# Optimization experiments

Hardware: AMD Instinct MI355X
Metric: run time of the kernel (lower is better)

## Reference

```python
import jax, jax.numpy as jnp
import numpy as np

SLOPE = 25.0   # snntorch surrogate.fast_sigmoid default slope
THR = 1.0      # snntorch Leaky default threshold
BETA = 0.95
SPIKE_STEPS = 4
NUM_HEADS = 16

@jax.custom_vjp
def spike(u):
    # Heaviside forward, fast-sigmoid surrogate backward
    return (u > 0).astype(u.dtype)

def _spike_fwd(u):
    return spike(u), u

def _spike_bwd(u, g):
    return (g / (SLOPE * jnp.abs(u) + 1.0) ** 2,)

spike.defvjp(_spike_fwd, _spike_bwd)

def lif_mean(cur):
    """Run SPIKE_STEPS of a snntorch Leaky neuron (subtract reset, detached)
    with constant input current `cur`; return mean spike train over time."""
    def step(mem, _):
        reset = jax.lax.stop_gradient(spike(mem - THR))
        mem = BETA * mem + cur - reset * THR
        return mem, spike(mem - THR)
    _, spk = jax.lax.scan(step, jnp.zeros_like(cur), None, length=SPIKE_STEPS)
    return spk.mean(axis=0)

def setup_inputs() -> dict:
    B, S, D = 2, 2048, 1024
    key = jax.random.key(0)
    ks = jax.random.split(key, 9)
    std = 1.0 / np.sqrt(D)
    mkw = lambda k: jax.random.uniform(k, (D, D), jnp.float32, -std, std)
    mkb = lambda k: jax.random.uniform(k, (D,), jnp.float32, -std, std)
    return {
        "x": jax.random.normal(ks[0], (B, S, D), jnp.float32),
        "q_w": mkw(ks[1]), "q_b": mkb(ks[2]),
        "k_w": mkw(ks[3]), "k_b": mkb(ks[4]),
        "v_w": mkw(ks[5]), "v_b": mkb(ks[6]),
        "o_w": mkw(ks[7]), "o_b": mkb(ks[8]),
    }

def reference(x, q_w, q_b, k_w, k_b, v_w, v_b, o_w, o_b):
    B, S, D = x.shape
    H = NUM_HEADS
    Hd = D // H
    # projections -> [B, H, S, Hd]  (weights stored [in, out])
    proj = lambda w, b: (x @ w + b).reshape(B, S, H, Hd).transpose(0, 2, 1, 3)
    q, k, v = proj(q_w, q_b), proj(k_w, k_b), proj(v_w, v_b)
    # LIF spiking recurrence, aggregated over time
    q_agg, k_agg, v_agg = lif_mean(q), lif_mean(k), lif_mean(v)
    # standard scaled dot-product attention on aggregated spikes
    scores = jnp.einsum('bhqd,bhkd->bhqk', q_agg, k_agg) / jnp.sqrt(jnp.float32(Hd))
    attn = jax.nn.softmax(scores, axis=-1)
    out = jnp.einsum('bhqk,bhkd->bhqd', attn, v_agg)
    out = out.transpose(0, 2, 1, 3).reshape(B, S, D)
    return out @ o_w + o_b
```

## Files before the change

kernel.cpp:

```cpp
#include <hip/hip_runtime.h>
#include <hip/hip_bf16.h>
#include <stdint.h>

typedef unsigned short u16;
typedef unsigned int u32;
typedef __bf16 bf16x8 __attribute__((ext_vector_type(8)));
typedef float f32x4 __attribute__((ext_vector_type(4)));

#define B_   2
#define S_   2048
#define D_   1024
#define H_   16
#define HD_  64

__device__ __forceinline__ u16 f2bf(float f) {
    u32 u = __float_as_uint(f);
    u32 r = (u + 0x7FFFu + ((u >> 16) & 1u)) >> 16;
    return (u16)r;
}
__device__ __forceinline__ float bf2f(u16 s) { return __uint_as_float(((u32)s) << 16); }

__device__ __forceinline__ f32x4 mfma16(bf16x8 a, bf16x8 b, f32x4 c) {
    return __builtin_amdgcn_mfma_f32_16x16x32_bf16(a, b, c, 0, 0, 0);
}

__device__ __forceinline__ void gl16(const u16* g, u16* l) {
    __builtin_amdgcn_global_load_lds(
        (const __attribute__((address_space(1))) void*)g,
        (__attribute__((address_space(3))) void*)l, 16, 0, 0);
}

__global__ void prep_kernel(const float* __restrict__ x,
                            const float* __restrict__ qw, const float* __restrict__ kw,
                            const float* __restrict__ vw, const float* __restrict__ ow,
                            u16* __restrict__ xbf, u16* __restrict__ wt_all) {
    __shared__ float tile[32][33];
    const int bid = blockIdx.x;
    const int t = threadIdx.x;
    if (bid < 4096) {
        int i = bid * 256 + t;
        float4 v = reinterpret_cast<const float4*>(x)[i];
        uint2 hp;
        hp.x = (u32)f2bf(v.x) | ((u32)f2bf(v.y) << 16);
        hp.y = (u32)f2bf(v.z) | ((u32)f2bf(v.w) << 16);
        reinterpret_cast<uint2*>(xbf)[i] = hp;
        return;
    }
    const int f = bid - 4096;
    const int z = f >> 10;
    const int bi = (f & 1023) >> 5;
    const int bj = f & 31;
    const float* w = (z == 0) ? qw : (z == 1) ? kw : (z == 2) ? vw : ow;
    u16* thi = wt_all + (size_t)z * 1048576;
    const int tx = t & 31, ty = t >> 5;
#pragma unroll
    for (int k = 0; k < 4; k++) {
        int r = ty + k * 8;
        tile[r][tx] = w[(size_t)(bi * 32 + r) * D_ + bj * 32 + tx];
    }
    __syncthreads();
#pragma unroll
    for (int k = 0; k < 4; k++) {
        int r = ty + k * 8;
        thi[(size_t)(bj * 32 + r) * D_ + bi * 32 + tx] = f2bf(tile[tx][r]);
    }
}

__global__ __launch_bounds__(256, 3)
void qkv_gemm(const u16* __restrict__ Ag, const u16* __restrict__ Bg,
              const float* __restrict__ qb, const float* __restrict__ kb,
              const float* __restrict__ vb,
              u16* __restrict__ o0, u16* __restrict__ o1, u16* __restrict__ o2) {
    __shared__ __align__(16) u16 lA[2][128 * 32];
    __shared__ __align__(16) u16 lB[2][128 * 32];

    const int t = threadIdx.x;
    const int flat = blockIdx.y * 24 + blockIdx.x;
    const int swz = (flat & 7) * 96 + (flat >> 3);
    const int m0 = (swz / 24) * 128;
    const int n0 = (swz % 24) * 128;
    const int wid = t >> 6, lane = t & 63;
    const int wm = wid >> 1, wn = wid & 1;
    const int lr = lane & 15, lg = lane >> 4;

    f32x4 acc[4][4] = {};

    auto STAGE = [&](int buf, int kk) {
        const int k0 = kk * 32;
#pragma unroll
        for (int p = 0; p < 2; p++) {
            int idx = p * 256 + wid * 64 + lane;
            int row = idx >> 2, sl = idx & 3;
            int slx = sl ^ ((row >> 1) & 3);
            gl16(Ag + (size_t)(m0 + row) * D_ + k0 + slx * 8,
                 &lA[buf][(p * 256 + wid * 64) * 8]);
            gl16(Bg + (size_t)(n0 + row) * D_ + k0 + slx * 8,
                 &lB[buf][(p * 256 + wid * 64) * 8]);
        }
    };

    STAGE(0, 0);
    __syncthreads();
    int cur = 0;

    for (int kk = 0; kk < 32; ++kk) {
        if (kk < 31) STAGE(cur ^ 1, kk + 1);

        bf16x8 af[4], bf[4];
#pragma unroll
        for (int m = 0; m < 4; m++) {
            int row = wm * 64 + m * 16 + lr;
            af[m] = *reinterpret_cast<const bf16x8*>(
                &lA[cur][row * 32 + (lg ^ ((row >> 1) & 3)) * 8]);
        }
#pragma unroll
        for (int n = 0; n < 4; n++) {
            int row = wn * 64 + n * 16 + lr;
            bf[n] = *reinterpret_cast<const bf16x8*>(
                &lB[cur][row * 32 + (lg ^ ((row >> 1) & 3)) * 8]);
        }
#pragma unroll
        for (int m = 0; m < 4; m++)
#pragma unroll
            for (int n = 0; n < 4; n++)
                acc[m][n] = mfma16(af[m], bf[n], acc[m][n]);

        __syncthreads();
        cur ^= 1;
    }

    const int col0f = n0 + wn * 64;
    const int proj = col0f >> 10;
    const float* bp = (proj == 0) ? qb : (proj == 1) ? kb : vb;
    u16* dst = (proj == 0) ? o0 : (proj == 1) ? o1 : o2;
#pragma unroll
    for (int m = 0; m < 4; m++) {
#pragma unroll
        for (int n = 0; n < 4; n++) {
            u16 agg4[4];
#pragma unroll
            for (int r = 0; r < 4; r++) {
                int row = m0 + wm * 64 + m * 16 + lg * 4 + r;
                int colp = (col0f + n * 16 + lr) & 1023;
                float cur_i = acc[m][n][r] + bp[colp];
                float mem = 0.f;
                int cnt = 0;
#pragma unroll
                for (int tt = 0; tt < 4; tt++) {
                    float reset = (mem > 1.f) ? 1.f : 0.f;
                    mem = 0.95f * mem;
                    mem = mem + cur_i;
                    mem = mem - reset;
                    cnt += (mem > 1.f) ? 1 : 0;
                }
                u16 agg = (u16)(__float_as_uint((float)cnt * 0.25f) >> 16);
                if (proj != 2) {
                    int b = row >> 11, s = row & 2047;
                    int h = colp >> 6, d = colp & 63;
                    dst[((size_t)(b * H_ + h) * S_ + s) * HD_ + d] = agg;
                } else {
                    agg4[r] = agg;
                }
            }
            if (proj == 2) {
                int row0 = m0 + wm * 64 + m * 16 + lg * 4;
                int colp = (col0f + n * 16 + lr) & 1023;
                int b = row0 >> 11, s = row0 & 2047;
                int h = colp >> 6, d = colp & 63;
                uint2 pk;
                pk.x = (u32)agg4[0] | ((u32)agg4[1] << 16);
                pk.y = (u32)agg4[2] | ((u32)agg4[3] << 16);
                *reinterpret_cast<uint2*>(
                    &dst[((size_t)(b * H_ + h) * HD_ + d) * S_ + s]) = pk;
            }
        }
    }
}

__global__ __launch_bounds__(256, 4)
void o_gemm(const u16* __restrict__ Ag, const u16* __restrict__ Bhg,
            const float* __restrict__ bias, float* __restrict__ out) {
    __shared__ __align__(16) u16 lA[2][64 * 32];
    __shared__ __align__(16) u16 lB[2][64 * 32];

    const int t = threadIdx.x;
    const int flat = blockIdx.y * 16 + blockIdx.x;
    const int swz = (flat & 7) * 128 + (flat >> 3);
    const int m0 = (swz >> 4) * 64;
    const int n0 = (swz & 15) * 64;
    const int wid = t >> 6, lane = t & 63;
    const int wm = wid >> 1, wn = wid & 1;
    const int lr = lane & 15, lg = lane >> 4;

    f32x4 acc[2][2] = {};

    auto STAGE = [&](int buf, int kk) {
        const int k0 = kk * 32;
        int idx = wid * 64 + lane;
        int row = idx >> 2, sl = idx & 3;
        int slx = sl ^ ((row >> 1) & 3);
        gl16(Ag + (size_t)(m0 + row) * D_ + k0 + slx * 8,
             &lA[buf][(wid * 64) * 8]);
        gl16(Bhg + (size_t)(n0 + row) * D_ + k0 + slx * 8,
             &lB[buf][(wid * 64) * 8]);
    };

    STAGE(0, 0);
    __syncthreads();
    int cur = 0;

    for (int kk = 0; kk < 32; ++kk) {
        if (kk < 31) STAGE(cur ^ 1, kk + 1);

        bf16x8 af[2], bf[2];
#pragma unroll
        for (int m = 0; m < 2; m++) {
            int row = wm * 32 + m * 16 + lr;
            af[m] = *reinterpret_cast<const bf16x8*>(
                &lA[cur][row * 32 + (lg ^ ((row >> 1) & 3)) * 8]);
        }
#pragma unroll
        for (int n = 0; n < 2; n++) {
            int row = wn * 32 + n * 16 + lr;
            bf[n] = *reinterpret_cast<const bf16x8*>(
                &lB[cur][row * 32 + (lg ^ ((row >> 1) & 3)) * 8]);
        }
#pragma unroll
        for (int m = 0; m < 2; m++)
#pragma unroll
            for (int n = 0; n < 2; n++)
                acc[m][n] = mfma16(af[m], bf[n], acc[m][n]);

        __syncthreads();
        cur ^= 1;
    }

#pragma unroll
    for (int m = 0; m < 2; m++)
#pragma unroll
        for (int n = 0; n < 2; n++)
#pragma unroll
            for (int r = 0; r < 4; r++) {
                int row = m0 + wm * 32 + m * 16 + lg * 4 + r;
                int col = n0 + wn * 32 + n * 16 + lr;
                out[(size_t)row * D_ + col] = acc[m][n][r] + bias[col];
            }
}

__global__ __launch_bounds__(256, 2)
void attn_kernel(const u16* __restrict__ qa, const u16* __restrict__ ka,
                 const u16* __restrict__ vt, u16* __restrict__ oag) {
    __shared__ __align__(16) u16 Kb[2][2][64 * 64];
    __shared__ __align__(16) u16 Vb[2][2][64 * 64];
    __shared__ __align__(16) u16 Pt[4][32 * 64];

    const int t = threadIdx.x;
    const int wid = t >> 6, lane = t & 63;
    const int lr = lane & 15, lg = lane >> 4;

    const int flat = blockIdx.y * 16 + blockIdx.x;
    const int swz = (flat & 7) * 64 + (flat >> 3);
    const int bh = swz >> 4;
    const int q0 = (swz & 15) * 128;

    const u16* qbase = qa + (size_t)bh * S_ * HD_;
    const u16* kbase = ka + (size_t)bh * S_ * HD_;
    const u16* vbase = vt + (size_t)bh * HD_ * S_;

    bf16x8 qf[2][2];
#pragma unroll
    for (int m = 0; m < 2; m++)
#pragma unroll
        for (int kc = 0; kc < 2; kc++) {
            int row = q0 + wid * 32 + m * 16 + lr;
            qf[m][kc] = *reinterpret_cast<const bf16x8*>(
                qbase + (size_t)row * HD_ + kc * 32 + lg * 8);
        }

    bf16x8 ones;
#pragma unroll
    for (int j = 0; j < 8; j++) ones[j] = (__bf16)1.0f;

    f32x4 oacc[2][4] = {};
    f32x4 ssum[2] = {};
    u16* myP = &Pt[wid][0];

    auto STAGE = [&](int buf, int kt2) {
#pragma unroll
        for (int s = 0; s < 2; s++) {
#pragma unroll
            for (int p = 0; p < 2; p++) {
                int slot = p * 256 + wid * 64 + lane;
                int row = slot >> 3, sl = slot & 7;
                int slx = sl ^ (row & 7);
                gl16(kbase + (size_t)((kt2 + s) * 64 + row) * HD_ + slx * 8,
                     &Kb[buf][s][(p * 256 + wid * 64) * 8]);
                gl16(vbase + (size_t)row * S_ + (kt2 + s) * 64 + slx * 8,
                     &Vb[buf][s][(p * 256 + wid * 64) * 8]);
            }
        }
    };

    auto COMPUTE = [&](const u16* Kt, const u16* Vt) {
        f32x4 sacc[2][4] = {};
        __builtin_amdgcn_s_setprio(1);
#pragma unroll
        for (int n = 0; n < 4; n++) {
            int row = n * 16 + lr;
#pragma unroll
            for (int kc = 0; kc < 2; kc++) {
                int sl = kc * 4 + lg;
                bf16x8 kb = *reinterpret_cast<const bf16x8*>(
                    &Kt[row * 64 + ((sl ^ (row & 7)) * 8)]);
                sacc[0][n] = mfma16(qf[0][kc], kb, sacc[0][n]);
                sacc[1][n] = mfma16(qf[1][kc], kb, sacc[1][n]);
            }
        }
        __builtin_amdgcn_s_setprio(0);
        char* pbase = reinterpret_cast<char*>(myP);
#pragma unroll
        for (int m = 0; m < 2; m++)
#pragma unroll
            for (int n = 0; n < 4; n++) {
                float pv[4];
#pragma unroll
                for (int r = 0; r < 4; r++) {
                    float tt = __builtin_fmaf(sacc[m][n][r], 0.18033688f,
                                              -5.7707802f);
                    asm("v_exp_f32 %0, %1" : "=v"(pv[r]) : "v"(tt));
                }
                u32 d01, d23;
                asm("v_cvt_pk_bf16_f32 %0, %1, %2"
                    : "=v"(d01) : "v"(pv[0]), "v"(pv[1]));
                asm("v_cvt_pk_bf16_f32 %0, %1, %2"
                    : "=v"(d23) : "v"(pv[2]), "v"(pv[3]));
                const int pr = m * 16 + lg * 4;
                const int cb = (n * 16 + lr) * 2;
                *reinterpret_cast<u16*>(pbase + (pr + 0) * 128 +
                                        (cb ^ (((pr + 0) & 7) << 4))) = (u16)d01;
                *reinterpret_cast<u16*>(pbase + (pr + 1) * 128 +
                                        (cb ^ (((pr + 1) & 7) << 4))) = (u16)(d01 >> 16);
                *reinterpret_cast<u16*>(pbase + (pr + 2) * 128 +
                                        (cb ^ (((pr + 2) & 7) << 4))) = (u16)d23;
                *reinterpret_cast<u16*>(pbase + (pr + 3) * 128 +
                                        (cb ^ (((pr + 3) & 7) << 4))) = (u16)(d23 >> 16);
            }
        bf16x8 pa[2][2];
#pragma unroll
        for (int m = 0; m < 2; m++)
#pragma unroll
            for (int kc = 0; kc < 2; kc++) {
                int row = m * 16 + lr;
                int sl = kc * 4 + lg;
                pa[m][kc] = *reinterpret_cast<const bf16x8*>(
                    &myP[row * 64 + ((sl ^ (row & 7)) * 8)]);
            }
        __builtin_amdgcn_s_setprio(1);
#pragma unroll
        for (int n = 0; n < 4; n++) {
            int row = n * 16 + lr;
#pragma unroll
            for (int kc = 0; kc < 2; kc++) {
                int sl = kc * 4 + lg;
                bf16x8 vb = *reinterpret_cast<const bf16x8*>(
                    &Vt[row * 64 + ((sl ^ (row & 7)) * 8)]);
                oacc[0][n] = mfma16(pa[0][kc], vb, oacc[0][n]);
                oacc[1][n] = mfma16(pa[1][kc], vb, oacc[1][n]);
            }
        }
        ssum[0] = mfma16(pa[0][0], ones, ssum[0]);
        ssum[0] = mfma16(pa[0][1], ones, ssum[0]);
        ssum[1] = mfma16(pa[1][0], ones, ssum[1]);
        ssum[1] = mfma16(pa[1][1], ones, ssum[1]);
        __builtin_amdgcn_s_setprio(0);
    };

    STAGE(0, 0);
    __syncthreads();
    int cur = 0;

    for (int pt = 0; pt < 16; ++pt) {
        if (pt < 15) STAGE(cur ^ 1, (pt + 1) * 2);
        COMPUTE(&Kb[cur][0][0], &Vb[cur][0][0]);
        COMPUTE(&Kb[cur][1][0], &Vb[cur][1][0]);
        __syncthreads();
        cur ^= 1;
    }

    const int b = bh >> 4, h = bh & 15;
#pragma unroll
    for (int m = 0; m < 2; m++)
#pragma unroll
        for (int n = 0; n < 4; n++)
#pragma unroll
            for (int r = 0; r < 4; r++) {
                int q = q0 + wid * 32 + m * 16 + lg * 4 + r;
                int d = n * 16 + lr;
                float v = oacc[m][n][r] / ssum[m][r];
                oag[(size_t)(b * S_ + q) * D_ + h * 64 + d] = f2bf(v);
            }
}

extern "C" void kernel_launch(void* const* d_in, const int* in_sizes, int n_in,
                              void* d_out, int out_size, void* d_ws, size_t ws_size,
                              hipStream_t stream) {
    (void)in_sizes; (void)n_in; (void)out_size; (void)ws_size;
    const float* x  = (const float*)d_in[0];
    const float* qw = (const float*)d_in[1];
    const float* qb = (const float*)d_in[2];
    const float* kw = (const float*)d_in[3];
    const float* kb = (const float*)d_in[4];
    const float* vw = (const float*)d_in[5];
    const float* vb = (const float*)d_in[6];
    const float* ow = (const float*)d_in[7];
    const float* ob = (const float*)d_in[8];

    u16* ws = (u16*)d_ws;
    const size_t C = 4194304;
    u16* xbf = ws + 0 * C;
    u16* wt  = ws + 1 * C;
    u16* qag = ws + 2 * C;
    u16* kag = ws + 3 * C;
    u16* vtg = ws + 4 * C;
    u16* oag = ws + 5 * C;

    prep_kernel<<<8192, 256, 0, stream>>>(x, qw, kw, vw, ow, xbf, wt);

    qkv_gemm<<<dim3(24, 32), 256, 0, stream>>>(
        xbf, wt, qb, kb, vb, qag, kag, vtg);
    attn_kernel<<<dim3(16, 32), 256, 0, stream>>>(qag, kag, vtg, oag);
    o_gemm<<<dim3(16, 64), 256, 0, stream>>>(
        oag, wt + 3 * 1048576, ob, (float*)d_out);
}
```

Before: 118.4 us.

## Triple-buffer GEMM loads and keep attention P in registers via 32x32 MFMA

Both projection GEMMs move from double to triple buffering. Each now waits on a partial vmcnt with a single barrier per k-step, so two tiles are in flight and one sync per iteration is dropped. The attention kernel switches to 32x32x16 MFMAs and computes S transposed, so the exponentiated probabilities can be packed and exchanged between lane halves with v_permlane32_swap. That removes the LDS round-trip for P and frees its shared-memory buffer. The risks are higher LDS usage in the GEMMs, which may lower occupancy, and more register pressure from the 16-wide accumulators.

New measurement: 109.4 us. -7.6%, faster.

```diff
diff --git a/kernel.cpp b/kernel.cpp
--- a/kernel.cpp
+++ b/kernel.cpp
@@ -6,6 +6,8 @@
 typedef unsigned int u32;
 typedef __bf16 bf16x8 __attribute__((ext_vector_type(8)));
 typedef float f32x4 __attribute__((ext_vector_type(4)));
+typedef float f32x16 __attribute__((ext_vector_type(16)));
+typedef u32 u32x4 __attribute__((ext_vector_type(4)));
 
 #define B_   2
 #define S_   2048
@@ -22,6 +24,9 @@
 
 __device__ __forceinline__ f32x4 mfma16(bf16x8 a, bf16x8 b, f32x4 c) {
     return __builtin_amdgcn_mfma_f32_16x16x32_bf16(a, b, c, 0, 0, 0);
+}
+__device__ __forceinline__ f32x16 mfma32(bf16x8 a, bf16x8 b, f32x16 c) {
+    return __builtin_amdgcn_mfma_f32_32x32x16_bf16(a, b, c, 0, 0, 0);
 }
 
 __device__ __forceinline__ void gl16(const u16* g, u16* l) {
@@ -71,8 +76,8 @@
               const float* __restrict__ qb, const float* __restrict__ kb,
               const float* __restrict__ vb,
               u16* __restrict__ o0, u16* __restrict__ o1, u16* __restrict__ o2) {
-    __shared__ __align__(16) u16 lA[2][128 * 32];
-    __shared__ __align__(16) u16 lB[2][128 * 32];
+    __shared__ __align__(16) u16 lA[3][128 * 32];
+    __shared__ __align__(16) u16 lB[3][128 * 32];
 
     const int t = threadIdx.x;
     const int flat = blockIdx.y * 24 + blockIdx.x;
@@ -100,12 +105,15 @@
     };
 
     STAGE(0, 0);
-    __syncthreads();
-    int cur = 0;
+    STAGE(1, 1);
 
     for (int kk = 0; kk < 32; ++kk) {
-        if (kk < 31) STAGE(cur ^ 1, kk + 1);
-
+        if (kk < 31) asm volatile("s_waitcnt vmcnt(4)" ::: "memory");
+        else         asm volatile("s_waitcnt vmcnt(0)" ::: "memory");
+        __builtin_amdgcn_s_barrier();
+        if (kk < 30) STAGE((kk + 2) % 3, kk + 2);
+
+        const int cur = kk % 3;
         bf16x8 af[4], bf[4];
 #pragma unroll
         for (int m = 0; m < 4; m++) {
@@ -124,9 +132,6 @@
 #pragma unroll
             for (int n = 0; n < 4; n++)
                 acc[m][n] = mfma16(af[m], bf[n], acc[m][n]);
-
-        __syncthreads();
-        cur ^= 1;
     }
 
     const int col0f = n0 + wn * 64;
@@ -180,8 +185,8 @@
 __global__ __launch_bounds__(256, 4)
 void o_gemm(const u16* __restrict__ Ag, const u16* __restrict__ Bhg,
             const float* __restrict__ bias, float* __restrict__ out) {
-    __shared__ __align__(16) u16 lA[2][64 * 32];
-    __shared__ __align__(16) u16 lB[2][64 * 32];
+    __shared__ __align__(16) u16 lA[3][64 * 32];
+    __shared__ __align__(16) u16 lB[3][64 * 32];
 
     const int t = threadIdx.x;
     const int flat = blockIdx.y * 16 + blockIdx.x;
@@ -206,12 +211,15 @@
     };
 
     STAGE(0, 0);
-    __syncthreads();
-    int cur = 0;
+    STAGE(1, 1);
 
     for (int kk = 0; kk < 32; ++kk) {
-        if (kk < 31) STAGE(cur ^ 1, kk + 1);
-
+        if (kk < 31) asm volatile("s_waitcnt vmcnt(2)" ::: "memory");
+        else         asm volatile("s_waitcnt vmcnt(0)" ::: "memory");
+        __builtin_amdgcn_s_barrier();
+        if (kk < 30) STAGE((kk + 2) % 3, kk + 2);
+
+        const int cur = kk % 3;
         bf16x8 af[2], bf[2];
 #pragma unroll
         for (int m = 0; m < 2; m++) {
@@ -230,9 +238,6 @@
 #pragma unroll
             for (int n = 0; n < 2; n++)
                 acc[m][n] = mfma16(af[m], bf[n], acc[m][n]);
-
-        __syncthreads();
-        cur ^= 1;
     }
 
 #pragma unroll
@@ -252,11 +257,11 @@
                  const u16* __restrict__ vt, u16* __restrict__ oag) {
     __shared__ __align__(16) u16 Kb[2][2][64 * 64];
     __shared__ __align__(16) u16 Vb[2][2][64 * 64];
-    __shared__ __align__(16) u16 Pt[4][32 * 64];
 
     const int t = threadIdx.x;
     const int wid = t >> 6, lane = t & 63;
-    const int lr = lane & 15, lg = lane >> 4;
+    const int l31 = lane & 31, hi = lane >> 5;
+    const int sx = l31 & 7;
 
     const int flat = blockIdx.y * 16 + blockIdx.x;
     const int swz = (flat & 7) * 64 + (flat >> 3);
@@ -267,23 +272,17 @@
     const u16* kbase = ka + (size_t)bh * S_ * HD_;
     const u16* vbase = vt + (size_t)bh * HD_ * S_;
 
-    bf16x8 qf[2][2];
-#pragma unroll
-    for (int m = 0; m < 2; m++)
-#pragma unroll
-        for (int kc = 0; kc < 2; kc++) {
-            int row = q0 + wid * 32 + m * 16 + lr;
-            qf[m][kc] = *reinterpret_cast<const bf16x8*>(
-                qbase + (size_t)row * HD_ + kc * 32 + lg * 8);
-        }
+    bf16x8 qf[4];
+#pragma unroll
+    for (int kc = 0; kc < 4; kc++)
+        qf[kc] = *reinterpret_cast<const bf16x8*>(
+            qbase + (size_t)(q0 + wid * 32 + l31) * HD_ + kc * 16 + hi * 8);
 
     bf16x8 ones;
 #pragma unroll
     for (int j = 0; j < 8; j++) ones[j] = (__bf16)1.0f;
 
-    f32x4 oacc[2][4] = {};
-    f32x4 ssum[2] = {};
-    u16* myP = &Pt[wid][0];
+    f32x16 oacc0 = {}, oacc1 = {}, ssum = {};
 
     auto STAGE = [&](int buf, int kt2) {
 #pragma unroll
@@ -302,76 +301,57 @@
     };
 
     auto COMPUTE = [&](const u16* Kt, const u16* Vt) {
-        f32x4 sacc[2][4] = {};
+        f32x16 sacc[2] = {};
         __builtin_amdgcn_s_setprio(1);
 #pragma unroll
-        for (int n = 0; n < 4; n++) {
-            int row = n * 16 + lr;
-#pragma unroll
-            for (int kc = 0; kc < 2; kc++) {
-                int sl = kc * 4 + lg;
-                bf16x8 kb = *reinterpret_cast<const bf16x8*>(
-                    &Kt[row * 64 + ((sl ^ (row & 7)) * 8)]);
-                sacc[0][n] = mfma16(qf[0][kc], kb, sacc[0][n]);
-                sacc[1][n] = mfma16(qf[1][kc], kb, sacc[1][n]);
-            }
+        for (int kc = 0; kc < 4; kc++) {
+            int sl = (2 * kc + hi) ^ sx;
+            bf16x8 k0 = *reinterpret_cast<const bf16x8*>(&Kt[l31 * 64 + sl * 8]);
+            bf16x8 k1 = *reinterpret_cast<const bf16x8*>(&Kt[(32 + l31) * 64 + sl * 8]);
+            sacc[0] = mfma32(k0, qf[kc], sacc[0]);
+            sacc[1] = mfma32(k1, qf[kc], sacc[1]);
         }
         __builtin_amdgcn_s_setprio(0);
-        char* pbase = reinterpret_cast<char*>(myP);
-#pragma unroll
-        for (int m = 0; m < 2; m++)
-#pragma unroll
-            for (int n = 0; n < 4; n++) {
-                float pv[4];
-#pragma unroll
-                for (int r = 0; r < 4; r++) {
-                    float tt = __builtin_fmaf(sacc[m][n][r], 0.18033688f,
-                                              -5.7707802f);
+        bf16x8 pa[4];
+#pragma unroll
+        for (int bb = 0; bb < 2; bb++) {
+#pragma unroll
+            for (int half = 0; half < 2; half++) {
+                float pv[8];
+#pragma unroll
+                for (int r = 0; r < 8; r++) {
+                    float tt = __builtin_fmaf(sacc[bb][half * 8 + r],
+                                              0.18033688f, -5.7707802f);
                     asm("v_exp_f32 %0, %1" : "=v"(pv[r]) : "v"(tt));
                 }
-                u32 d01, d23;
+                u32 A1, A2, B1, B2;
                 asm("v_cvt_pk_bf16_f32 %0, %1, %2"
-                    : "=v"(d01) : "v"(pv[0]), "v"(pv[1]));
+                    : "=v"(A1) : "v"(pv[0]), "v"(pv[1]));
                 asm("v_cvt_pk_bf16_f32 %0, %1, %2"
-                    : "=v"(d23) : "v"(pv[2]), "v"(pv[3]));
-                const int pr = m * 16 + lg * 4;
-                const int cb = (n * 16 + lr) * 2;
-                *reinterpret_cast<u16*>(pbase + (pr + 0) * 128 +
-                                        (cb ^ (((pr + 0) & 7) << 4))) = (u16)d01;
-                *reinterpret_cast<u16*>(pbase + (pr + 1) * 128 +
-                                        (cb ^ (((pr + 1) & 7) << 4))) = (u16)(d01 >> 16);
-                *reinterpret_cast<u16*>(pbase + (pr + 2) * 128 +
-                                        (cb ^ (((pr + 2) & 7) << 4))) = (u16)d23;
-                *reinterpret_cast<u16*>(pbase + (pr + 3) * 128 +
-                                        (cb ^ (((pr + 3) & 7) << 4))) = (u16)(d23 >> 16);
+                    : "=v"(A2) : "v"(pv[2]), "v"(pv[3]));
+                asm("v_cvt_pk_bf16_f32 %0, %1, %2"
+                    : "=v"(B1) : "v"(pv[4]), "v"(pv[5]));
+                asm("v_cvt_pk_bf16_f32 %0, %1, %2"
+                    : "=v"(B2) : "v"(pv[6]), "v"(pv[7]));
+                asm("v_permlane32_swap_b32 %0, %1" : "+v"(A1), "+v"(B1));
+                asm("v_permlane32_swap_b32 %0, %1" : "+v"(A2), "+v"(B2));
+                u32x4 pw;
+                pw.x = A1; pw.y = A2; pw.z = B1; pw.w = B2;
+                pa[bb * 2 + half] = __builtin_bit_cast(bf16x8, pw);
             }
-        bf16x8 pa[2][2];
-#pragma unroll
-        for (int m = 0; m < 2; m++)
-#pragma unroll
-            for (int kc = 0; kc < 2; kc++) {
-                int row = m * 16 + lr;
-                int sl = kc * 4 + lg;
-                pa[m][kc] = *reinterpret_cast<const bf16x8*>(
-                    &myP[row * 64 + ((sl ^ (row & 7)) * 8)]);
-            }
+        }
         __builtin_amdgcn_s_setprio(1);
 #pragma unroll
-        for (int n = 0; n < 4; n++) {
-            int row = n * 16 + lr;
-#pragma unroll
-            for (int kc = 0; kc < 2; kc++) {
-                int sl = kc * 4 + lg;
-                bf16x8 vb = *reinterpret_cast<const bf16x8*>(
-                    &Vt[row * 64 + ((sl ^ (row & 7)) * 8)]);
-                oacc[0][n] = mfma16(pa[0][kc], vb, oacc[0][n]);
-                oacc[1][n] = mfma16(pa[1][kc], vb, oacc[1][n]);
-            }
-        }
-        ssum[0] = mfma16(pa[0][0], ones, ssum[0]);
-        ssum[0] = mfma16(pa[0][1], ones, ssum[0]);
-        ssum[1] = mfma16(pa[1][0], ones, ssum[1]);
-        ssum[1] = mfma16(pa[1][1], ones, ssum[1]);
+        for (int k4 = 0; k4 < 4; k4++)
+            ssum = mfma32(pa[k4], ones, ssum);
+#pragma unroll
+        for (int k4 = 0; k4 < 4; k4++) {
+            int sl = (2 * k4 + hi) ^ sx;
+            bf16x8 v0 = *reinterpret_cast<const bf16x8*>(&Vt[l31 * 64 + sl * 8]);
+            bf16x8 v1 = *reinterpret_cast<const bf16x8*>(&Vt[(32 + l31) * 64 + sl * 8]);
+            oacc0 = mfma32(pa[k4], v0, oacc0);
+            oacc1 = mfma32(pa[k4], v1, oacc1);
+        }
         __builtin_amdgcn_s_setprio(0);
     };
 
@@ -389,16 +369,14 @@
 
     const int b = bh >> 4, h = bh & 15;
 #pragma unroll
-    for (int m = 0; m < 2; m++)
-#pragma unroll
-        for (int n = 0; n < 4; n++)
-#pragma unroll
-            for (int r = 0; r < 4; r++) {
-                int q = q0 + wid * 32 + m * 16 + lg * 4 + r;
-                int d = n * 16 + lr;
-                float v = oacc[m][n][r] / ssum[m][r];
-                oag[(size_t)(b * S_ + q) * D_ + h * 64 + d] = f2bf(v);
-            }
+    for (int r = 0; r < 16; r++) {
+        int q = q0 + wid * 32 + (r & 3) + 8 * (r >> 2) + 4 * hi;
+        size_t base = (size_t)(b * S_ + q) * D_ + h * 64;
+        float v0 = oacc0[r] / ssum[r];
+        float v1 = oacc1[r] / ssum[r];
+        oag[base + l31] = f2bf(v0);
+        oag[base + 32 + l31] = f2bf(v1);
+    }
 }
 
 extern "C" void kernel_launch(void* const* d_in, const int* in_sizes, int n_in,
```
